# Optimization experiments

Measured on AMD Instinct MI355X. Metric: run time of the kernel, lower is better.

The kernel has to match this reference:

```python
import jax, jax.numpy as jnp
import numpy as np

B, T, D, H, V = 32, 1024, 768, 1024, 30522
TAU_RANK, GAMMA_RANK, TAU_GATE = 0.05, 2.0, 0.2
RHOS = (0.1, 0.25, 0.5)


def setup_inputs() -> dict:
    key = jax.random.key(0)
    ks = jax.random.split(key, 6)
    ids = jax.random.randint(ks[0], (B, T), 0, V, dtype=jnp.int32)
    embeddings = jax.random.normal(ks[1], (B, T, D), dtype=jnp.float32)
    attn = jax.random.randint(ks[2], (B, T), 0, 2, dtype=jnp.int32)
    return {
        'ids': ids,
        'embeddings': embeddings,
        'attn': attn,
        'ln_g': jnp.ones((D,), jnp.float32),
        'ln_b': jnp.zeros((D,), jnp.float32),
        'w1': jax.random.normal(ks[3], (D, H), jnp.float32) * 0.02,
        'b1': jnp.zeros((H,), jnp.float32),
        'w2': jax.random.normal(ks[4], (H, 1), jnp.float32) * 0.02,
        'b2': jnp.zeros((1,), jnp.float32),
        'emb_table': jax.random.normal(ks[5], (V, D), jnp.float32) * 0.02,
    }


def _layer_norm(x, g, b, eps=1e-5):
    mu = x.mean(-1, keepdims=True)
    var = ((x - mu) ** 2).mean(-1, keepdims=True)
    return (x - mu) * jax.lax.rsqrt(var + eps) * g + b


def _selector(x, ln_g, ln_b, w1, b1, w2, b2):
    # SelectorMLP (dropout in eval mode): LN -> Linear -> exact GELU -> Linear -> squeeze
    h = _layer_norm(x, ln_g, ln_b)
    h = jax.nn.gelu(h @ w1 + b1, approximate=False)
    return (h @ w2 + b2)[..., 0]  # [B,T]


def _soft_rank(scores, attn_f, tau, gamma):
    scores = jnp.where(attn_f == 0, 0.0, scores)
    denom = jnp.clip(attn_f.sum(1, keepdims=True), 1.0, None)
    mean = (scores * attn_f).sum(1, keepdims=True) / denom
    var = (((scores - mean) ** 2) * attn_f).sum(1, keepdims=True) / denom
    scores = (scores - mean) / jnp.sqrt(var + 1e-6)
    # diff[b,i,j] = scores[b,j] - scores[b,i]
    diff = scores[:, None, :] - scores[:, :, None]
    p = jax.nn.sigmoid(diff / tau) ** gamma
    p = p * attn_f[:, None, :]
    r = 1.0 + p.sum(axis=1)  # [B,T]
    return jnp.where(attn_f == 0, 1e9, r)


def _pool(tok, w):
    # masked weighted mean pooling (stub of sent_encoder.pool)
    return (tok * w[:, :, None]).sum(1) / jnp.clip(w.sum(1), 1e-9, None)[:, None]


def reference(ids, embeddings, attn, ln_g, ln_b, w1, b1, w2, b2, emb_table):
    attn_f = attn.astype(jnp.float32)
    emb = embeddings * attn_f[..., None]
    scores = _selector(emb, ln_g, ln_b, w1, b1, w2, b2)
    scores = jnp.where(attn_f == 0, 0.0, scores)

    tok_full = emb_table[ids]  # stub sent_encoder.token_embeddings
    full_rep = jax.lax.stop_gradient(_pool(tok_full, attn_f))  # torch.no_grad()

    T_eff = attn_f.sum(1)
    ranks = _soft_rank(scores, attn_f, TAU_RANK, GAMMA_RANK)
    # position of each token in ascending rank order; padded tokens (rank 1e9) sort last
    pos = jnp.argsort(jnp.argsort(ranks, axis=1), axis=1)

    recon_sum = jnp.zeros((), jnp.float32)
    hard_masks, rho_effs, losses = [], [], []
    for rho in RHOS:
        k = jnp.maximum(jnp.round(rho * T_eff), 1.0)  # per-batch variable k
        gate_raw = jax.nn.sigmoid((k[:, None] - ranks) / TAU_GATE) * attn_f
        g_soft = gate_raw / jnp.clip(gate_raw.sum(1, keepdims=True), 1e-8, None) * k[:, None]
        # batched equivalent of the per-row topk(-ranks, kb) scatter loop
        hard_mask = (pos < k[:, None]).astype(jnp.float32)
        k_eff = g_soft.sum(1)
        rho_eff = k_eff / jnp.clip(T_eff, 1.0, None)
        effective_attn = attn_f * g_soft
        pred_rep = _pool(emb_table[ids], effective_attn)
        l_r = jnp.mean((pred_rep - full_rep) ** 2)  # recon_loss stub (MSE)
        recon_sum = recon_sum + l_r
        hard_masks.append(hard_mask)
        rho_effs.append(rho_eff)
        losses.append(l_r)
    recon_avg = recon_sum / len(RHOS)
    return (g_soft, jnp.stack(hard_masks), recon_avg, jnp.stack(losses), jnp.stack(rho_effs))
```

## Files before the change

### kernel.cpp

```cpp
#include <hip/hip_runtime.h>
#include <math.h>

#define BT 32768
#define Dd 768
#define Hh 1024
#define Bb 32
#define Tt 1024
#define MT_CAP 17152
#define MTILE_CAP 134

typedef __bf16 bf16x8 __attribute__((ext_vector_type(8)));
typedef float f32x4 __attribute__((ext_vector_type(4)));

#define GL2LDS16(gp, lp) __builtin_amdgcn_global_load_lds( \
    (const __attribute__((address_space(1))) void*)(gp),   \
    (__attribute__((address_space(3))) void*)(lp), 16, 0, 0)

__device__ __forceinline__ float block_reduce_sum_256(float v, float* red4) {
    int tid = threadIdx.x;
    #pragma unroll
    for (int o = 32; o > 0; o >>= 1) v += __shfl_down(v, o);
    __syncthreads();
    if ((tid & 63) == 0) red4[tid >> 6] = v;
    __syncthreads();
    return red4[0] + red4[1] + red4[2] + red4[3];
}

__device__ __forceinline__ void bf16split(float x, short& h, short& l) {
    unsigned u = __float_as_uint(x);
    unsigned r = (u + 0x7FFFu + ((u >> 16) & 1u)) >> 16;
    h = (short)r;
    float fh = __uint_as_float(r << 16);
    float lof = x - fh;
    unsigned u2 = __float_as_uint(lof);
    unsigned r2 = (u2 + 0x7FFFu + ((u2 >> 16) & 1u)) >> 16;
    l = (short)r2;
}

__device__ __forceinline__ int pack2(short a, short b) {
    return (int)(unsigned short)a | ((int)(unsigned short)b << 16);
}

__global__ __launch_bounds__(256) void seg_count_kernel(
    const int* __restrict__ attn, int* __restrict__ segsum)
{
    const int tid = threadIdx.x;
    int a = (attn[blockIdx.x * 256 + tid] != 0) ? 1 : 0;
    #pragma unroll
    for (int o = 32; o > 0; o >>= 1) a += __shfl_down(a, o);
    __shared__ int w4[4];
    if ((tid & 63) == 0) w4[tid >> 6] = a;
    __syncthreads();
    if (tid == 0) segsum[blockIdx.x] = w4[0] + w4[1] + w4[2] + w4[3];
}

__global__ __launch_bounds__(256) void cidx_kernel(
    const int* __restrict__ attn, const int* __restrict__ segsum,
    const float* __restrict__ b2,
    int* __restrict__ row_of, int* __restrict__ tok_of,
    float* __restrict__ scores, float* __restrict__ teff, int* __restrict__ mh)
{
    __shared__ int sbase[128];
    __shared__ int w0tot;
    __shared__ int wcnt[4];
    const int bid = blockIdx.x, tid = threadIdx.x;

    int v = 0, s = 0;
    if (tid < 128) {
        const int ln = tid & 63;
        v = segsum[tid];
        s = v;
        #pragma unroll
        for (int o = 1; o < 64; o <<= 1) {
            int t = __shfl_up(s, o);
            if (ln >= o) s += t;
        }
        if (tid == 63) w0tot = s;
    }
    __syncthreads();
    if (tid < 128) {
        int base = (tid >= 64) ? w0tot : 0;
        sbase[tid] = base + s - v;
        if (tid == 127 && bid == 0) mh[0] = base + s;
    }
    if (tid == 0 && (bid & 3) == 0)
        teff[bid >> 2] = (float)(segsum[bid] + segsum[bid + 1] +
                                 segsum[bid + 2] + segsum[bid + 3]);

    const int tok = bid * 256 + tid;
    const int active = (attn[tok] != 0) ? 1 : 0;
    unsigned long long m = __ballot(active);
    const int lane = tid & 63, wv = tid >> 6;
    if (lane == 0) wcnt[wv] = __popcll(m);
    __syncthreads();
    int woff = 0;
    for (int q = 0; q < wv; ++q) woff += wcnt[q];
    int below = __popcll(m & ((1ULL << lane) - 1ULL));
    int row = sbase[bid] + woff + below;
    row_of[tok] = active ? row : -1;
    if (active) tok_of[row] = tok;
    scores[tok] = active ? b2[0] : 0.f;
}

__global__ __launch_bounds__(256) void prep_a_kernel(
    const float* __restrict__ emb, const int* __restrict__ attn,
    const int* __restrict__ row_of,
    const float* __restrict__ ln_g, const float* __restrict__ ln_b,
    short* __restrict__ a_hi, short* __restrict__ a_lo)
{
    int tok  = blockIdx.x * 4 + (threadIdx.x >> 6);
    int lane = threadIdx.x & 63;
    int av   = attn[tok];
    if (av == 0) return;
    int row = row_of[tok];
    if (row >= MT_CAP) return;
    float af = (float)av;
    const float4* row4 = (const float4*)(emb + (size_t)tok * Dd);
    float4 x[3];
    #pragma unroll
    for (int e = 0; e < 3; ++e) x[e] = row4[lane + 64 * e];
    float s = 0.f;
    #pragma unroll
    for (int e = 0; e < 3; ++e) {
        x[e].x *= af; x[e].y *= af; x[e].z *= af; x[e].w *= af;
        s += x[e].x + x[e].y + x[e].z + x[e].w;
    }
    #pragma unroll
    for (int o = 32; o > 0; o >>= 1) s += __shfl_down(s, o);
    s = __shfl(s, 0);
    float mean = s / 768.0f;
    float q = 0.f;
    #pragma unroll
    for (int e = 0; e < 3; ++e) {
        float d0 = x[e].x - mean, d1 = x[e].y - mean, d2 = x[e].z - mean, d3 = x[e].w - mean;
        q += d0*d0 + d1*d1 + d2*d2 + d3*d3;
    }
    #pragma unroll
    for (int o = 32; o > 0; o >>= 1) q += __shfl_down(q, o);
    q = __shfl(q, 0);
    float rstd = 1.0f / sqrtf(q / 768.0f + 1e-5f);

    #pragma unroll
    for (int e = 0; e < 3; ++e) {
        int idx = lane * 4 + e * 256;
        float4 g4 = *(const float4*)(ln_g + idx);
        float4 b4 = *(const float4*)(ln_b + idx);
        float o0 = (x[e].x - mean) * rstd * g4.x + b4.x;
        float o1 = (x[e].y - mean) * rstd * g4.y + b4.y;
        float o2 = (x[e].z - mean) * rstd * g4.z + b4.z;
        float o3 = (x[e].w - mean) * rstd * g4.w + b4.w;
        short h0,h1,h2,h3,l0,l1,l2,l3;
        bf16split(o0,h0,l0); bf16split(o1,h1,l1);
        bf16split(o2,h2,l2); bf16split(o3,h3,l3);
        *(int2*)(a_hi + (size_t)row * 768 + idx) = make_int2(pack2(h0,h1), pack2(h2,h3));
        *(int2*)(a_lo + (size_t)row * 768 + idx) = make_int2(pack2(l0,l1), pack2(l2,l3));
    }
}

__global__ __launch_bounds__(256) void prep_w1t_kernel(
    const float* __restrict__ w1, short* __restrict__ w1t_hi, short* __restrict__ w1t_lo)
{
    __shared__ float tile[32][65];
    const int kb  = blockIdx.x % 24;
    const int nb0 = (blockIdx.x / 24) * 64;
    const int tid = threadIdx.x;
    const int r0 = tid >> 6, c = tid & 63;
    #pragma unroll
    for (int rr = 0; rr < 8; ++rr) {
        int k = kb * 32 + r0 + rr * 4;
        tile[r0 + rr * 4][c] = w1[(size_t)k * 1024 + nb0 + c];
    }
    __syncthreads();
    const int n = tid >> 2, kc = (tid & 3) * 8;
    short h[8], lo[8];
    #pragma unroll
    for (int e = 0; e < 8; ++e) bf16split(tile[kc + e][n], h[e], lo[e]);
    size_t off = (size_t)(nb0 + n) * 768 + kb * 32 + kc;
    *(int4*)(w1t_hi + off) = make_int4(pack2(h[0],h[1]), pack2(h[2],h[3]),
                                       pack2(h[4],h[5]), pack2(h[6],h[7]));
    *(int4*)(w1t_lo + off) = make_int4(pack2(lo[0],lo[1]), pack2(lo[2],lo[3]),
                                       pack2(lo[4],lo[5]), pack2(lo[6],lo[7]));
}

__global__ __launch_bounds__(512, 4) void score_gemm_mfma(
    const __bf16* __restrict__ a_hi, const __bf16* __restrict__ a_lo,
    const __bf16* __restrict__ w1t_hi, const __bf16* __restrict__ w1t_lo,
    const float* __restrict__ b1, const float* __restrict__ w2,
    const int* __restrict__ mh, const int* __restrict__ tok_of,
    float* __restrict__ scores)
{
    const int Mh = mh[0];
    int MtAct = (Mh + 127) >> 7;
    if (MtAct > MTILE_CAP) MtAct = MTILE_CAP;
    const int MtPad8 = (MtAct + 7) & ~7;
    const int njobs  = MtPad8 * 8;
    const int job = blockIdx.x;
    if (job >= njobs) return;
    const int mt = job % MtPad8;
    const int m0 = mt * 128;
    if (m0 >= Mh) return;
    const int nc = job / MtPad8;
    const int nb = nc * 128;

    __shared__ __align__(16) __bf16 sAh[2][8][512];
    __shared__ __align__(16) __bf16 sAl[2][8][512];
    __shared__ __align__(16) __bf16 sBh[2][8][512];
    __shared__ __align__(16) __bf16 sBl[2][8][512];

    const int tid = threadIdx.x;
    const int l   = tid & 63;
    const int w   = tid >> 6;
    const int rsel = l & 15;
    const int ksel = (l >> 4) * 8;
    const int wr   = w >> 2, wc = w & 3;

    const size_t aA = (size_t)(m0 + w * 16 + rsel) * 768 + ksel;
    const size_t aB = (size_t)(nb + w * 16 + rsel) * 768 + ksel;

    f32x4 acc[4][2];
    #pragma unroll
    for (int i = 0; i < 4; ++i)
        #pragma unroll
        for (int j = 0; j < 2; ++j) acc[i][j] = (f32x4){0.f, 0.f, 0.f, 0.f};

    auto stage = [&](int buf, int k0) {
        GL2LDS16(a_hi   + aA + k0, &sAh[buf][w][0]);
        GL2LDS16(a_lo   + aA + k0, &sAl[buf][w][0]);
        GL2LDS16(w1t_hi + aB + k0, &sBh[buf][w][0]);
        GL2LDS16(w1t_lo + aB + k0, &sBl[buf][w][0]);
    };

    stage(0, 0);

    for (int kt = 0; kt < 24; ++kt) {
        const int cur = kt & 1;
        __syncthreads();
        if (kt < 23) stage(cur ^ 1, (kt + 1) * 32);

        bf16x8 ah[4], al[4], bh[2], bl[2];
        #pragma unroll
        for (int mi = 0; mi < 4; ++mi) {
            ah[mi] = *(const bf16x8*)&sAh[cur][wr * 4 + mi][l * 8];
            al[mi] = *(const bf16x8*)&sAl[cur][wr * 4 + mi][l * 8];
        }
        #pragma unroll
        for (int ni = 0; ni < 2; ++ni) {
            bh[ni] = *(const bf16x8*)&sBh[cur][wc * 2 + ni][l * 8];
            bl[ni] = *(const bf16x8*)&sBl[cur][wc * 2 + ni][l * 8];
        }
        #pragma unroll
        for (int mi = 0; mi < 4; ++mi)
            #pragma unroll
            for (int ni = 0; ni < 2; ++ni)
                acc[mi][ni] = __builtin_amdgcn_mfma_f32_16x16x32_bf16(ah[mi], bh[ni], acc[mi][ni], 0, 0, 0);
        #pragma unroll
        for (int mi = 0; mi < 4; ++mi)
            #pragma unroll
            for (int ni = 0; ni < 2; ++ni)
                acc[mi][ni] = __builtin_amdgcn_mfma_f32_16x16x32_bf16(al[mi], bh[ni], acc[mi][ni], 0, 0, 0);
        #pragma unroll
        for (int mi = 0; mi < 4; ++mi)
            #pragma unroll
            for (int ni = 0; ni < 2; ++ni)
                acc[mi][ni] = __builtin_amdgcn_mfma_f32_16x16x32_bf16(ah[mi], bl[ni], acc[mi][ni], 0, 0, 0);
    }

    const int colbase = nb + wc * 32 + (l & 15);
    const int rowg    = (l >> 4) * 4;
    #pragma unroll
    for (int mi = 0; mi < 4; ++mi) {
        float v[4] = {0.f, 0.f, 0.f, 0.f};
        #pragma unroll
        for (int ni = 0; ni < 2; ++ni) {
            int col = colbase + ni * 16;
            float b1v = b1[col], w2v = w2[col];
            #pragma unroll
            for (int j = 0; j < 4; ++j) {
                float x = acc[mi][ni][j] + b1v;
                float g = 0.5f * x * (1.0f + erff(x * 0.70710678118654752440f));
                v[j] = fmaf(g, w2v, v[j]);
            }
        }
        #pragma unroll
        for (int j = 0; j < 4; ++j) {
            v[j] += __shfl_xor(v[j], 1);
            v[j] += __shfl_xor(v[j], 2);
            v[j] += __shfl_xor(v[j], 4);
            v[j] += __shfl_xor(v[j], 8);
        }
        if ((l & 15) == 0) {
            int rowb = m0 + wr * 64 + mi * 16 + rowg;
            #pragma unroll
            for (int j = 0; j < 4; ++j) {
                int row = rowb + j;
                if (row < Mh) atomicAdd(&scores[tok_of[row]], v[j]);
            }
        }
    }
}

__global__ __launch_bounds__(256) void rank_kernel(
    const float* __restrict__ scores, const int* __restrict__ attn,
    float* __restrict__ ranks, int* __restrict__ pos)
{
    __shared__ float sn[1024];
    __shared__ float afs[1024];
    __shared__ double dsum[256];
    __shared__ int    csum[256];
    __shared__ float  red4[4];
    const int b = blockIdx.x >> 4, qc = blockIdx.x & 15;
    const int tid = threadIdx.x;

    float sv[4], av[4];
    float sa = 0.f, ss = 0.f;
    #pragma unroll
    for (int e = 0; e < 4; ++e) {
        int i = tid + 256 * e;
        float af = (float)attn[b * 1024 + i];
        float s  = (af != 0.f) ? scores[b * 1024 + i] : 0.f;
        sn[i]  = s;
        afs[i] = af;
        sv[e] = s; av[e] = af;
        sa += af; ss += s;
    }
    float tot_a = block_reduce_sum_256(sa, red4);
    float tot_s = block_reduce_sum_256(ss, red4);
    float denom = fmaxf(tot_a, 1.0f);
    float mean  = tot_s / denom;
    float q = 0.f;
    #pragma unroll
    for (int e = 0; e < 4; ++e) { float d = sv[e] - mean; q += d * d * av[e]; }
    float tot_q = block_reduce_sum_256(q, red4);
    float rinv  = 1.0f / sqrtf(tot_q / denom + 1e-6f);

    #pragma unroll
    for (int e = 0; e < 4; ++e) {
        int i = tid + 256 * e;
        sn[i] = (sn[i] - mean) * rinv;
    }
    __syncthreads();

    const int jj = tid & 63;
    const int qt = tid >> 6;
    const int j  = qc * 64 + jj;
    const float sj = sn[j];
    const bool  aj = (afs[j] != 0.f);
    double sum = 0.0;
    int    cnt = 0;
    const int i0 = qt * 256;
    #pragma unroll 4
    for (int i = i0; i < i0 + 256; ++i) {
        float si = sn[i];
        float ai = afs[i];
        float d   = (sj - si) * 20.0f;
        float ee  = expf(-fabsf(d));
        float rcp = 1.0f / (1.0f + ee);
        float sig = (d >= 0.f) ? rcp : ee * rcp;
        sum += (double)(sig * sig);
        bool c;
        if (ai != 0.f) c = aj ? (si < sj || (si == sj && i < j)) : true;
        else           c = aj ? false : (i < j);
        cnt += c ? 1 : 0;
    }
    dsum[tid] = sum; csum[tid] = cnt;
    __syncthreads();
    if (tid < 64) {
        double s2 = dsum[tid] + dsum[tid + 64] + dsum[tid + 128] + dsum[tid + 192];
        int    c2 = csum[tid] + csum[tid + 64] + csum[tid + 128] + csum[tid + 192];
        int gj = b * 1024 + qc * 64 + tid;
        ranks[gj] = (afs[qc * 64 + tid] == 0.f) ? 1e9f : (float)(1.0 + s2);
        pos[gj]   = c2;
    }
}

__global__ __launch_bounds__(256) void gate_kernel(
    const float* __restrict__ ranks, const int* __restrict__ attn,
    const float* __restrict__ teff_v, const int* __restrict__ pos,
    float* __restrict__ w_rho, float* __restrict__ keff, float* __restrict__ out)
{
    __shared__ float red4[4];
    const int b = blockIdx.x / 3, r = blockIdx.x % 3;
    const int tid = threadIdx.x;
    const float teff = teff_v[b];
    const float rhos[3] = {0.1f, 0.25f, 0.5f};
    const float k = fmaxf(rintf(rhos[r] * teff), 1.0f);
    float rj[4], afj[4];
    int pj[4];
    float gate[4]; float lsum = 0.f;
    #pragma unroll
    for (int e = 0; e < 4; ++e) {
        int j = tid + 256 * e;
        rj[e]  = ranks[b * 1024 + j];
        afj[e] = (float)attn[b * 1024 + j];
        pj[e]  = pos[b * 1024 + j];
        float d   = (k - rj[e]) / 0.2f;
        float ee  = expf(-fabsf(d));
        float rcp = 1.0f / (1.0f + ee);
        float sig = (d >= 0.f) ? rcp : ee * rcp;
        gate[e] = sig * afj[e];
        lsum += gate[e];
    }
    float gsum = block_reduce_sum_256(lsum, red4);
    float cl   = fmaxf(gsum, 1e-8f);
    float ls2  = 0.f;
    #pragma unroll
    for (int e = 0; e < 4; ++e) {
        int j = tid + 256 * e;
        float gs = gate[e] / cl * k;
        ls2 += gs;
        w_rho[r * BT + b * 1024 + j]     = gs;
        out[BT + r * BT + b * 1024 + j]  = ((float)pj[e] < k) ? 1.0f : 0.0f;
        if (r == 2) out[b * 1024 + j] = gs;
    }
    float ks = block_reduce_sum_256(ls2, red4);
    if (tid == 0) {
        keff[r * Bb + b] = ks;
        out[131076 + r * Bb + b] = ks / fmaxf(teff, 1.0f);
    }
}

__global__ __launch_bounds__(256) void pool_kernel(
    const int* __restrict__ ids, const int* __restrict__ attn,
    const float* __restrict__ emb_table, const float* __restrict__ w_rho,
    float* __restrict__ ppart)
{
    const int b = blockIdx.x >> 4, chunk = blockIdx.x & 15;
    const int tid = threadIdx.x;
    float accF[3] = {0,0,0}, acc0[3] = {0,0,0}, acc1[3] = {0,0,0}, acc2[3] = {0,0,0};
    const int t0 = chunk * 64;
    for (int t = t0; t < t0 + 64; ++t) {
        int gi = b * 1024 + t;
        if (attn[gi] == 0) continue;
        float w0 = w_rho[gi], wa = w_rho[BT + gi], wb = w_rho[2 * BT + gi];
        const float* row = emb_table + (size_t)ids[gi] * 768;
        #pragma unroll
        for (int e = 0; e < 3; ++e) {
            float v = row[tid + 256 * e];
            accF[e] += v;
            acc0[e] = fmaf(w0, v, acc0[e]);
            acc1[e] = fmaf(wa, v, acc1[e]);
            acc2[e] = fmaf(wb, v, acc2[e]);
        }
    }
    float* base = ppart + ((size_t)chunk * 4 * Bb + b) * 768;
    #pragma unroll
    for (int e = 0; e < 3; ++e) {
        int d = tid + 256 * e;
        base[0 * Bb * 768 + d] = acc0[e];
        base[1 * Bb * 768 + d] = acc1[e];
        base[2 * Bb * 768 + d] = acc2[e];
        base[3 * Bb * 768 + d] = accF[e];
    }
}

__global__ __launch_bounds__(256) void final96_kernel(
    const float* __restrict__ ppart, const float* __restrict__ keff,
    const float* __restrict__ teff_v, float* __restrict__ part)
{
    __shared__ float red4[4];
    const int b = blockIdx.x / 3, r = blockIdx.x % 3;
    const int tid = threadIdx.x;
    const float kinv = 1.0f / fmaxf(keff[r * Bb + b], 1e-9f);
    const float tinv = 1.0f / fmaxf(teff_v[b], 1e-9f);
    float local = 0.f;
    for (int d = tid; d < 768; d += 256) {
        float pr = 0.f, fu = 0.f;
        #pragma unroll
        for (int c = 0; c < 16; ++c) {
            pr += ppart[(size_t)c * 98304 + (r * Bb + b) * 768 + d];
            fu += ppart[(size_t)c * 98304 + (3 * Bb + b) * 768 + d];
        }
        float df = pr * kinv - fu * tinv;
        local += df * df;
    }
    float tot = block_reduce_sum_256(local, red4);
    if (tid == 0) part[r * 32 + b] = tot;
}

__global__ void final_avg_kernel(const float* __restrict__ part, float* __restrict__ out) {
    __shared__ float sp[96];
    const int tid = threadIdx.x;
    if (tid < 96) sp[tid] = part[tid];
    __syncthreads();
    if (tid == 0) {
        float l0 = 0.f, l1 = 0.f, l2 = 0.f;
        #pragma unroll
        for (int b = 0; b < 32; ++b) { l0 += sp[b]; l1 += sp[32 + b]; l2 += sp[64 + b]; }
        l0 /= 24576.0f; l1 /= 24576.0f; l2 /= 24576.0f;
        out[131073] = l0;
        out[131074] = l1;
        out[131075] = l2;
        out[131072] = (l0 + l1 + l2) / 3.0f;
    }
}

extern "C" void kernel_launch(void* const* d_in, const int* in_sizes, int n_in,
                              void* d_out, int out_size, void* d_ws, size_t ws_size,
                              hipStream_t stream) {
    const int*   ids       = (const int*)d_in[0];
    const float* emb       = (const float*)d_in[1];
    const int*   attn      = (const int*)d_in[2];
    const float* ln_g      = (const float*)d_in[3];
    const float* ln_b      = (const float*)d_in[4];
    const float* w1        = (const float*)d_in[5];
    const float* b1        = (const float*)d_in[6];
    const float* w2        = (const float*)d_in[7];
    const float* b2        = (const float*)d_in[8];
    const float* emb_table = (const float*)d_in[9];
    float* out = (float*)d_out;
    float* ws  = (float*)d_ws;

    float* scores = ws;
    float* ranks  = ws + 32768;
    float* w_rho  = ws + 65536;
    float* teff   = ws + 163840;
    float* part   = ws + 163872;
    float* keff   = ws + 163968;
    int*   pos    = (int*)(ws + 164096);
    int*   row_of = (int*)(ws + 196864);
    int*   tok_of = (int*)(ws + 229632);
    int*   segsum = (int*)(ws + 262400);
    int*   mh     = (int*)(ws + 262528);
    short* a_hi   = (short*)(ws + 262592);
    short* a_lo   = a_hi + (size_t)MT_CAP * 768;
    short* w1t_hi = a_lo + (size_t)MT_CAP * 768;
    short* w1t_lo = w1t_hi + 1024 * 768;
    float* ppart  = (float*)a_hi;

    seg_count_kernel<<<128, 256, 0, stream>>>(attn, segsum);
    cidx_kernel<<<128, 256, 0, stream>>>(attn, segsum, b2, row_of, tok_of,
                                         scores, teff, mh);
    prep_w1t_kernel<<<384, 256, 0, stream>>>(w1, w1t_hi, w1t_lo);
    prep_a_kernel<<<8192, 256, 0, stream>>>(emb, attn, row_of, ln_g, ln_b, a_hi, a_lo);

    score_gemm_mfma<<<1088, 512, 0, stream>>>(
        (const __bf16*)a_hi, (const __bf16*)a_lo,
        (const __bf16*)w1t_hi, (const __bf16*)w1t_lo,
        b1, w2, mh, tok_of, scores);

    rank_kernel<<<512, 256, 0, stream>>>(scores, attn, ranks, pos);
    gate_kernel<<<96, 256, 0, stream>>>(ranks, attn, teff, pos, w_rho, keff, out);
    pool_kernel<<<512, 256, 0, stream>>>(ids, attn, emb_table, w_rho, ppart);
    final96_kernel<<<96, 256, 0, stream>>>(ppart, keff, teff, part);
    final_avg_kernel<<<1, 128, 0, stream>>>(part, out);
}
```

Baseline: 228.8 us.

## Fuse prep kernels, split rank work finer, fold gating into pooling kernel

Merges the w1 transpose/split and activation prep into one launch, doubles rank_kernel blocks (32 columns × 8 row groups) with a cheaper sigmoid via __expf, and has rank_kernel emit per-chunk gate partial sums. The gate computation then moves into the pooling kernel, which rebuilds the normalized gates in shared memory instead of reading w_rho from global memory. This removes two launches and the w_rho round trip but recomputes the gate sums in every pool block and changes the sigmoid numerics slightly.

Result: faster. 207.3 us (median of 3 runs) (-9.4%).

```diff
diff --git a/kernel.cpp b/kernel.cpp
--- a/kernel.cpp
+++ b/kernel.cpp
@@ -102,14 +102,41 @@
     scores[tok] = active ? b2[0] : 0.f;
 }
 
-__global__ __launch_bounds__(256) void prep_a_kernel(
+__global__ __launch_bounds__(256) void prep_kernel(
+    const float* __restrict__ w1,
+    short* __restrict__ w1t_hi, short* __restrict__ w1t_lo,
     const float* __restrict__ emb, const int* __restrict__ attn,
     const int* __restrict__ row_of,
     const float* __restrict__ ln_g, const float* __restrict__ ln_b,
     short* __restrict__ a_hi, short* __restrict__ a_lo)
 {
-    int tok  = blockIdx.x * 4 + (threadIdx.x >> 6);
-    int lane = threadIdx.x & 63;
+    __shared__ float tile[32][65];
+    const int bid = blockIdx.x, tid = threadIdx.x;
+
+    if (bid < 384) {
+        const int kb  = bid % 24;
+        const int nb0 = (bid / 24) * 64;
+        const int r0 = tid >> 6, c = tid & 63;
+        #pragma unroll
+        for (int rr = 0; rr < 8; ++rr) {
+            int k = kb * 32 + r0 + rr * 4;
+            tile[r0 + rr * 4][c] = w1[(size_t)k * 1024 + nb0 + c];
+        }
+        __syncthreads();
+        const int n = tid >> 2, kc = (tid & 3) * 8;
+        short h[8], lo[8];
+        #pragma unroll
+        for (int e = 0; e < 8; ++e) bf16split(tile[kc + e][n], h[e], lo[e]);
+        size_t off = (size_t)(nb0 + n) * 768 + kb * 32 + kc;
+        *(int4*)(w1t_hi + off) = make_int4(pack2(h[0],h[1]), pack2(h[2],h[3]),
+                                           pack2(h[4],h[5]), pack2(h[6],h[7]));
+        *(int4*)(w1t_lo + off) = make_int4(pack2(lo[0],lo[1]), pack2(lo[2],lo[3]),
+                                           pack2(lo[4],lo[5]), pack2(lo[6],lo[7]));
+        return;
+    }
+
+    int tok  = (bid - 384) * 4 + (tid >> 6);
+    int lane = tid & 63;
     int av   = attn[tok];
     if (av == 0) return;
     int row = row_of[tok];
@@ -157,31 +184,6 @@
     }
 }
 
-__global__ __launch_bounds__(256) void prep_w1t_kernel(
-    const float* __restrict__ w1, short* __restrict__ w1t_hi, short* __restrict__ w1t_lo)
-{
-    __shared__ float tile[32][65];
-    const int kb  = blockIdx.x % 24;
-    const int nb0 = (blockIdx.x / 24) * 64;
-    const int tid = threadIdx.x;
-    const int r0 = tid >> 6, c = tid & 63;
-    #pragma unroll
-    for (int rr = 0; rr < 8; ++rr) {
-        int k = kb * 32 + r0 + rr * 4;
-        tile[r0 + rr * 4][c] = w1[(size_t)k * 1024 + nb0 + c];
-    }
-    __syncthreads();
-    const int n = tid >> 2, kc = (tid & 3) * 8;
-    short h[8], lo[8];
-    #pragma unroll
-    for (int e = 0; e < 8; ++e) bf16split(tile[kc + e][n], h[e], lo[e]);
-    size_t off = (size_t)(nb0 + n) * 768 + kb * 32 + kc;
-    *(int4*)(w1t_hi + off) = make_int4(pack2(h[0],h[1]), pack2(h[2],h[3]),
-                                       pack2(h[4],h[5]), pack2(h[6],h[7]));
-    *(int4*)(w1t_lo + off) = make_int4(pack2(lo[0],lo[1]), pack2(lo[2],lo[3]),
-                                       pack2(lo[4],lo[5]), pack2(lo[6],lo[7]));
-}
-
 __global__ __launch_bounds__(512, 4) void score_gemm_mfma(
     const __bf16* __restrict__ a_hi, const __bf16* __restrict__ a_lo,
     const __bf16* __restrict__ w1t_hi, const __bf16* __restrict__ w1t_lo,
@@ -301,14 +303,14 @@
 
 __global__ __launch_bounds__(256) void rank_kernel(
     const float* __restrict__ scores, const int* __restrict__ attn,
-    float* __restrict__ ranks, int* __restrict__ pos)
+    float* __restrict__ ranks, int* __restrict__ pos, float* __restrict__ gpart)
 {
     __shared__ float sn[1024];
     __shared__ float afs[1024];
     __shared__ double dsum[256];
     __shared__ int    csum[256];
     __shared__ float  red4[4];
-    const int b = blockIdx.x >> 4, qc = blockIdx.x & 15;
+    const int b = blockIdx.x >> 5, qc = blockIdx.x & 31;
     const int tid = threadIdx.x;
 
     float sv[4], av[4];
@@ -340,22 +342,21 @@
     }
     __syncthreads();
 
-    const int jj = tid & 63;
-    const int qt = tid >> 6;
-    const int j  = qc * 64 + jj;
+    const int jj  = tid & 31;
+    const int grp = tid >> 5;
+    const int j   = qc * 32 + jj;
     const float sj = sn[j];
     const bool  aj = (afs[j] != 0.f);
     double sum = 0.0;
     int    cnt = 0;
-    const int i0 = qt * 256;
+    const int i0 = grp * 128;
     #pragma unroll 4
-    for (int i = i0; i < i0 + 256; ++i) {
+    for (int i = i0; i < i0 + 128; ++i) {
         float si = sn[i];
         float ai = afs[i];
         float d   = (sj - si) * 20.0f;
-        float ee  = expf(-fabsf(d));
-        float rcp = 1.0f / (1.0f + ee);
-        float sig = (d >= 0.f) ? rcp : ee * rcp;
+        float e   = __expf(-d);
+        float sig = 1.0f / (1.0f + e);
         sum += (double)(sig * sig);
         bool c;
         if (ai != 0.f) c = aj ? (si < sj || (si == sj && i < j)) : true;
@@ -364,74 +365,85 @@
     }
     dsum[tid] = sum; csum[tid] = cnt;
     __syncthreads();
-    if (tid < 64) {
-        double s2 = dsum[tid] + dsum[tid + 64] + dsum[tid + 128] + dsum[tid + 192];
-        int    c2 = csum[tid] + csum[tid + 64] + csum[tid + 128] + csum[tid + 192];
-        int gj = b * 1024 + qc * 64 + tid;
-        ranks[gj] = (afs[qc * 64 + tid] == 0.f) ? 1e9f : (float)(1.0 + s2);
+    if (tid < 32) {
+        double s2 = 0.0; int c2 = 0;
+        #pragma unroll
+        for (int g = 0; g < 8; ++g) { s2 += dsum[tid + 32 * g]; c2 += csum[tid + 32 * g]; }
+        const int jt = qc * 32 + tid;
+        const int gj = b * 1024 + jt;
+        const float af = afs[jt];
+        const float rk = (af == 0.f) ? 1e9f : (float)(1.0 + s2);
+        ranks[gj] = rk;
         pos[gj]   = c2;
-    }
-}
-
-__global__ __launch_bounds__(256) void gate_kernel(
-    const float* __restrict__ ranks, const int* __restrict__ attn,
-    const float* __restrict__ teff_v, const int* __restrict__ pos,
-    float* __restrict__ w_rho, float* __restrict__ keff, float* __restrict__ out)
-{
-    __shared__ float red4[4];
-    const int b = blockIdx.x / 3, r = blockIdx.x % 3;
-    const int tid = threadIdx.x;
-    const float teff = teff_v[b];
-    const float rhos[3] = {0.1f, 0.25f, 0.5f};
-    const float k = fmaxf(rintf(rhos[r] * teff), 1.0f);
-    float rj[4], afj[4];
-    int pj[4];
-    float gate[4]; float lsum = 0.f;
-    #pragma unroll
-    for (int e = 0; e < 4; ++e) {
-        int j = tid + 256 * e;
-        rj[e]  = ranks[b * 1024 + j];
-        afj[e] = (float)attn[b * 1024 + j];
-        pj[e]  = pos[b * 1024 + j];
-        float d   = (k - rj[e]) / 0.2f;
-        float ee  = expf(-fabsf(d));
-        float rcp = 1.0f / (1.0f + ee);
-        float sig = (d >= 0.f) ? rcp : ee * rcp;
-        gate[e] = sig * afj[e];
-        lsum += gate[e];
-    }
-    float gsum = block_reduce_sum_256(lsum, red4);
-    float cl   = fmaxf(gsum, 1e-8f);
-    float ls2  = 0.f;
-    #pragma unroll
-    for (int e = 0; e < 4; ++e) {
-        int j = tid + 256 * e;
-        float gs = gate[e] / cl * k;
-        ls2 += gs;
-        w_rho[r * BT + b * 1024 + j]     = gs;
-        out[BT + r * BT + b * 1024 + j]  = ((float)pj[e] < k) ? 1.0f : 0.0f;
-        if (r == 2) out[b * 1024 + j] = gs;
-    }
-    float ks = block_reduce_sum_256(ls2, red4);
-    if (tid == 0) {
-        keff[r * Bb + b] = ks;
-        out[131076 + r * Bb + b] = ks / fmaxf(teff, 1.0f);
-    }
-}
-
-__global__ __launch_bounds__(256) void pool_kernel(
+        const float rhos[3] = {0.1f, 0.25f, 0.5f};
+        #pragma unroll
+        for (int r = 0; r < 3; ++r) {
+            float k = fmaxf(rintf(rhos[r] * tot_a), 1.0f);
+            float d = (k - rk) * 5.0f;
+            float g = (1.0f / (1.0f + __expf(-d))) * af;
+            #pragma unroll
+            for (int o = 16; o > 0; o >>= 1) g += __shfl_xor(g, o);
+            if (tid == 0) gpart[b * 96 + r * 32 + qc] = g;
+        }
+    }
+}
+
+__global__ __launch_bounds__(256) void gate_pool_kernel(
     const int* __restrict__ ids, const int* __restrict__ attn,
-    const float* __restrict__ emb_table, const float* __restrict__ w_rho,
-    float* __restrict__ ppart)
-{
+    const float* __restrict__ emb_table,
+    const float* __restrict__ ranks, const int* __restrict__ pos,
+    const float* __restrict__ gpart, const float* __restrict__ teff_v,
+    float* __restrict__ keff, float* __restrict__ ppart, float* __restrict__ out)
+{
+    __shared__ float gpl[96];
+    __shared__ float gsL[3][64];
     const int b = blockIdx.x >> 4, chunk = blockIdx.x & 15;
     const int tid = threadIdx.x;
+    const int t0 = chunk * 64;
+    const float teff = teff_v[b];
+
+    if (tid < 96) gpl[tid] = gpart[b * 96 + tid];
+    __syncthreads();
+
+    const float rhos[3] = {0.1f, 0.25f, 0.5f};
+    float kk[3], gsum[3], scale[3];
+    #pragma unroll
+    for (int r = 0; r < 3; ++r) {
+        float s = 0.f;
+        #pragma unroll
+        for (int c = 0; c < 32; ++c) s += gpl[r * 32 + c];
+        gsum[r]  = s;
+        kk[r]    = fmaxf(rintf(rhos[r] * teff), 1.0f);
+        scale[r] = kk[r] / fmaxf(s, 1e-8f);
+    }
+
+    if (tid < 192) {
+        const int r = tid >> 6, t = tid & 63;
+        const int gj = b * 1024 + t0 + t;
+        const float rk = ranks[gj];
+        const float af = (float)attn[gj];
+        float d    = (kk[r] - rk) * 5.0f;
+        float gate = (1.0f / (1.0f + __expf(-d))) * af;
+        float gs   = gate * scale[r];
+        gsL[r][t] = gs;
+        out[BT + r * BT + gj] = ((float)pos[gj] < kk[r]) ? 1.0f : 0.0f;
+        if (r == 2) out[gj] = gs;
+    }
+    if (chunk == 0 && tid == 0) {
+        #pragma unroll
+        for (int r = 0; r < 3; ++r) {
+            float ke = kk[r] * (gsum[r] / fmaxf(gsum[r], 1e-8f));
+            keff[r * Bb + b] = ke;
+            out[131076 + r * Bb + b] = ke / fmaxf(teff, 1.0f);
+        }
+    }
+    __syncthreads();
+
     float accF[3] = {0,0,0}, acc0[3] = {0,0,0}, acc1[3] = {0,0,0}, acc2[3] = {0,0,0};
-    const int t0 = chunk * 64;
     for (int t = t0; t < t0 + 64; ++t) {
         int gi = b * 1024 + t;
         if (attn[gi] == 0) continue;
-        float w0 = w_rho[gi], wa = w_rho[BT + gi], wb = w_rho[2 * BT + gi];
+        float w0 = gsL[0][t - t0], wa = gsL[1][t - t0], wb = gsL[2][t - t0];
         const float* row = emb_table + (size_t)ids[gi] * 768;
         #pragma unroll
         for (int e = 0; e < 3; ++e) {
@@ -512,16 +524,16 @@
 
     float* scores = ws;
     float* ranks  = ws + 32768;
-    float* w_rho  = ws + 65536;
-    float* teff   = ws + 163840;
-    float* part   = ws + 163872;
-    float* keff   = ws + 163968;
-    int*   pos    = (int*)(ws + 164096);
-    int*   row_of = (int*)(ws + 196864);
-    int*   tok_of = (int*)(ws + 229632);
-    int*   segsum = (int*)(ws + 262400);
-    int*   mh     = (int*)(ws + 262528);
-    short* a_hi   = (short*)(ws + 262592);
+    float* teff   = ws + 65536;
+    float* part   = ws + 65568;
+    float* keff   = ws + 65664;
+    float* gpart  = ws + 65760;
+    int*   pos    = (int*)(ws + 68864);
+    int*   row_of = (int*)(ws + 101632);
+    int*   tok_of = (int*)(ws + 134400);
+    int*   segsum = (int*)(ws + 167168);
+    int*   mh     = (int*)(ws + 167296);
+    short* a_hi   = (short*)(ws + 167360);
     short* a_lo   = a_hi + (size_t)MT_CAP * 768;
     short* w1t_hi = a_lo + (size_t)MT_CAP * 768;
     short* w1t_lo = w1t_hi + 1024 * 768;
@@ -530,17 +542,17 @@
     seg_count_kernel<<<128, 256, 0, stream>>>(attn, segsum);
     cidx_kernel<<<128, 256, 0, stream>>>(attn, segsum, b2, row_of, tok_of,
                                          scores, teff, mh);
-    prep_w1t_kernel<<<384, 256, 0, stream>>>(w1, w1t_hi, w1t_lo);
-    prep_a_kernel<<<8192, 256, 0, stream>>>(emb, attn, row_of, ln_g, ln_b, a_hi, a_lo);
+    prep_kernel<<<8576, 256, 0, stream>>>(w1, w1t_hi, w1t_lo,
+                                          emb, attn, row_of, ln_g, ln_b, a_hi, a_lo);
 
     score_gemm_mfma<<<1088, 512, 0, stream>>>(
         (const __bf16*)a_hi, (const __bf16*)a_lo,
         (const __bf16*)w1t_hi, (const __bf16*)w1t_lo,
         b1, w2, mh, tok_of, scores);
 
-    rank_kernel<<<512, 256, 0, stream>>>(scores, attn, ranks, pos);
-    gate_kernel<<<96, 256, 0, stream>>>(ranks, attn, teff, pos, w_rho, keff, out);
-    pool_kernel<<<512, 256, 0, stream>>>(ids, attn, emb_table, w_rho, ppart);
+    rank_kernel<<<1024, 256, 0, stream>>>(scores, attn, ranks, pos, gpart);
+    gate_pool_kernel<<<512, 256, 0, stream>>>(ids, attn, emb_table, ranks, pos,
+                                              gpart, teff, keff, ppart, out);
     final96_kernel<<<96, 256, 0, stream>>>(ppart, keff, teff, part);
     final_avg_kernel<<<1, 128, 0, stream>>>(part, out);
 }
```
